# Optimization experiments

Hardware: AMD Instinct MI355X
Metric: run time of the kernel (lower is better)

## Reference

```python
import jax, jax.numpy as jnp
import numpy as np

N = 50000   # nodes
E = 600000  # edges (avg degree 12)
D = 128     # feature dim (input=hidden=output)
L = 3       # GIN layers
BN_EPS = 1e-5


def _bn(x, g, b):
    # BatchNorm1d in training mode: per-feature batch mean / biased variance
    m = jnp.mean(x, axis=0)
    v = jnp.var(x, axis=0)
    return (x - m) * jax.lax.rsqrt(v + BN_EPS) * g + b


def setup_inputs() -> dict:
    key = jax.random.key(0)
    ks = jax.random.split(key, 5)
    h = jax.random.normal(ks[0], (N, D), jnp.float32)
    edges = jax.random.randint(ks[1], (2, E), 0, N, dtype=jnp.int32)
    w = jax.random.uniform(ks[2], (E,), jnp.float32)
    scale = 1.0 / np.sqrt(D)
    W0s = jax.random.normal(ks[3], (L, D, D), jnp.float32) * scale
    W1s = jax.random.normal(ks[4], (L, D, D), jnp.float32) * scale
    ones = jnp.ones((L, D), jnp.float32)
    zeros = jnp.zeros((L, D), jnp.float32)
    return dict(h=h, edges=edges, w=w, W0s=W0s, W1s=W1s,
                bn1_g=ones, bn1_b=zeros,   # MLP internal BN
                bn2_g=ones, bn2_b=zeros,   # ApplyNodeFunc BN
                bn3_g=ones, bn3_b=zeros)   # outer GIN BN


def reference(h, edges, w, W0s, W1s, bn1_g, bn1_b, bn2_g, bn2_b, bn3_g, bn3_b):
    src, dst = edges[0], edges[1]
    for i in range(L):
        # GINConv, sum pooling, eps = 0: (1+eps)*h + sum_{j in N(v)} w_ij * h_j
        agg = jax.ops.segment_sum(h[src] * w[:, None], dst, num_segments=N)
        x = h + agg
        # ApplyNodeFunc: MLP (lin -> BN -> relu -> lin), then BN, relu
        x = jax.nn.relu(_bn(x @ W0s[i], bn1_g[i], bn1_b[i]))
        x = x @ W1s[i]
        x = jax.nn.relu(_bn(x, bn2_g[i], bn2_b[i]))
        # outer per-layer BatchNorm; relu except on the last layer
        h = _bn(x, bn3_g[i], bn3_b[i])
        if i != L - 1:
            h = jax.nn.relu(h)
    return h
```

## Files before the change

kernel.cpp:

```cpp
#include <hip/hip_runtime.h>
#include <stdint.h>

#define NN 50000
#define EE 600000
#define DD 128
#define LL 3
#define NB 196
#define NBANK 16
#define SB (NBANK * 256)
#define GA 3125

typedef __attribute__((ext_vector_type(8))) short short8;
typedef __attribute__((ext_vector_type(4))) float f32x4;
typedef __attribute__((ext_vector_type(4))) unsigned int u32x4;

static __device__ __forceinline__ ushort f2bf(float f) {
    uint32_t u = __builtin_bit_cast(uint32_t, f);
    u += 0x7FFFu + ((u >> 16) & 1u);
    return (ushort)(u >> 16);
}
static __device__ __forceinline__ float bf2f(ushort u) {
    uint32_t x = ((uint32_t)u) << 16;
    return __builtin_bit_cast(float, x);
}
static __device__ __forceinline__ float bflo(uint32_t p) { return bf2f((ushort)(p & 0xffffu)); }
static __device__ __forceinline__ float bfhi(uint32_t p) { return bf2f((ushort)(p >> 16)); }

static __device__ __forceinline__ void gload_lds16(const void* g, void* l) {
    __builtin_amdgcn_global_load_lds(
        (const __attribute__((address_space(1))) uint32_t*)g,
        (__attribute__((address_space(3))) uint32_t*)l, 16, 0, 0);
}

static __device__ __forceinline__ float2 bank_sum(const float* st, int t) {
    float s1 = 0.f, s2 = 0.f;
    #pragma unroll
    for (int bb = 0; bb < NBANK; ++bb) {
        s1 += st[bb * 256 + t];
        s2 += st[bb * 256 + DD + t];
    }
    return make_float2(s1, s2);
}

__global__ __launch_bounds__(256) void prep_w(
    const float* __restrict__ W0s, const float* __restrict__ W1s,
    ushort* __restrict__ wt, int* __restrict__ deg, float* __restrict__ stats)
{
    __shared__ float ws[8192];
    const int b = blockIdx.x;
    const int t = threadIdx.x;

    {
        int i = b * 256 + t;
        if (i < NN) deg[i] = 0;
        if (b >= 12 && b < 12 + 9 * NBANK) stats[(b - 12) * 256 + t] = 0.f;
    }

    if (b < 12) {
        const int m = b >> 1, kh = b & 1;
        const float* W = (m < 3 ? W0s + (size_t)m * 16384
                                : W1s + (size_t)(m - 3) * 16384) + (size_t)kh * 64 * 128;
        #pragma unroll
        for (int i = 0; i < 8; ++i) {
            int i4 = t + i * 256;
            reinterpret_cast<float4*>(ws)[i4] = reinterpret_cast<const float4*>(W)[i4];
        }
        __syncthreads();
        ushort* out = wt + (size_t)m * 16384;
        const int j = t & 127;
        const int rep = t >> 7;
        #pragma unroll
        for (int si = 0; si < 4; ++si) {
            int s = kh * 8 + rep * 4 + si;
            int kloc = (rep * 4 + si) * 8;
            short8 pk;
            #pragma unroll
            for (int q = 0; q < 8; ++q) pk[q] = (short)f2bf(ws[(kloc + q) * 128 + j]);
            int slot = s ^ (j & 7);
            *reinterpret_cast<short8*>(out + j * 128 + slot * 8) = pk;
        }
    }
}

__global__ __launch_bounds__(256) void hist_kernel(
    const int* __restrict__ dst, int* __restrict__ deg)
{
    int e = blockIdx.x * 256 + threadIdx.x;
    if (e < EE) atomicAdd(&deg[dst[e]], 1);
}

__global__ __launch_bounds__(256) void scan_a(
    const int* __restrict__ deg, int* __restrict__ partials)
{
    int i = blockIdx.x * 256 + threadIdx.x;
    int v = (i < NN) ? deg[i] : 0;
    #pragma unroll
    for (int d = 1; d < 64; d <<= 1) v += __shfl_xor(v, d);
    __shared__ int wsum[4];
    if ((threadIdx.x & 63) == 0) wsum[threadIdx.x >> 6] = v;
    __syncthreads();
    if (threadIdx.x == 0)
        partials[blockIdx.x] = wsum[0] + wsum[1] + wsum[2] + wsum[3];
}

__global__ __launch_bounds__(256) void scan_c(
    const int* __restrict__ deg, const int* __restrict__ partials,
    int* __restrict__ off, int* __restrict__ cursor)
{
    __shared__ int ps[256], s[256];
    const int t = threadIdx.x;
    int pv = (t < NB) ? partials[t] : 0;
    ps[t] = pv;
    __syncthreads();
    for (int d = 1; d < 256; d <<= 1) {
        int u = (t >= d) ? ps[t - d] : 0;
        __syncthreads();
        ps[t] += u;
        __syncthreads();
    }
    int base = (blockIdx.x > 0) ? ps[blockIdx.x - 1] : 0;

    int i = blockIdx.x * 256 + t;
    int v = (i < NN) ? deg[i] : 0;
    s[t] = v;
    __syncthreads();
    for (int d = 1; d < 256; d <<= 1) {
        int u = (t >= d) ? s[t - d] : 0;
        __syncthreads();
        s[t] += u;
        __syncthreads();
    }
    int excl = base + s[t] - v;
    if (i < NN) { off[i] = excl; cursor[i] = excl; }
    if (i == 0) off[NN] = EE;
}

__global__ __launch_bounds__(256) void binsort_kernel(
    const int* __restrict__ src, const int* __restrict__ dst,
    const float* __restrict__ w, int* __restrict__ cursor,
    int2* __restrict__ em)
{
    int e = blockIdx.x * 256 + threadIdx.x;
    if (e >= EE) return;
    int d = dst[e];
    int p = atomicAdd(&cursor[d], 1);
    em[p] = make_int2(src[e], __float_as_int(w[e]));
}

__global__ __launch_bounds__(256) void gather_kernel(
    const ushort* __restrict__ y0, const int* __restrict__ off,
    const long long* __restrict__ em, ushort* __restrict__ y,
    float* __restrict__ st0)
{
    __shared__ float red[4][256];
    const int t = threadIdx.x;
    const int wave = t >> 6, lane = t & 63;
    const int qw = lane >> 4, ql = lane & 15;
    const int v = blockIdx.x * 16 + wave * 4 + qw;

    const int beg = off[v], end = off[v + 1];
    const ushort* rowbase = y0 + ql * 8;

    uint4 sw = *reinterpret_cast<const uint4*>(y0 + (size_t)v * DD + ql * 8);
    float a0 = bflo(sw.x), a1 = bfhi(sw.x), a2 = bflo(sw.y), a3 = bfhi(sw.y);
    float a4 = bflo(sw.z), a5 = bfhi(sw.z), a6 = bflo(sw.w), a7 = bfhi(sw.w);

    int j = beg;
    for (; j + 3 < end; j += 4) {
        long long q0 = __builtin_nontemporal_load(&em[j]);
        long long q1 = __builtin_nontemporal_load(&em[j + 1]);
        long long q2 = __builtin_nontemporal_load(&em[j + 2]);
        long long q3 = __builtin_nontemporal_load(&em[j + 3]);
        int s0 = (int)(q0 & 0xffffffffLL), s1 = (int)(q1 & 0xffffffffLL);
        int s2 = (int)(q2 & 0xffffffffLL), s3 = (int)(q3 & 0xffffffffLL);
        float w0 = __int_as_float((int)(q0 >> 32)), w1 = __int_as_float((int)(q1 >> 32));
        float w2 = __int_as_float((int)(q2 >> 32)), w3 = __int_as_float((int)(q3 >> 32));
        uint4 p0 = *reinterpret_cast<const uint4*>(rowbase + (size_t)s0 * DD);
        uint4 p1 = *reinterpret_cast<const uint4*>(rowbase + (size_t)s1 * DD);
        uint4 p2 = *reinterpret_cast<const uint4*>(rowbase + (size_t)s2 * DD);
        uint4 p3 = *reinterpret_cast<const uint4*>(rowbase + (size_t)s3 * DD);
        a0 = fmaf(w0, bflo(p0.x), a0); a1 = fmaf(w0, bfhi(p0.x), a1);
        a2 = fmaf(w0, bflo(p0.y), a2); a3 = fmaf(w0, bfhi(p0.y), a3);
        a4 = fmaf(w0, bflo(p0.z), a4); a5 = fmaf(w0, bfhi(p0.z), a5);
        a6 = fmaf(w0, bflo(p0.w), a6); a7 = fmaf(w0, bfhi(p0.w), a7);
        a0 = fmaf(w1, bflo(p1.x), a0); a1 = fmaf(w1, bfhi(p1.x), a1);
        a2 = fmaf(w1, bflo(p1.y), a2); a3 = fmaf(w1, bfhi(p1.y), a3);
        a4 = fmaf(w1, bflo(p1.z), a4); a5 = fmaf(w1, bfhi(p1.z), a5);
        a6 = fmaf(w1, bflo(p1.w), a6); a7 = fmaf(w1, bfhi(p1.w), a7);
        a0 = fmaf(w2, bflo(p2.x), a0); a1 = fmaf(w2, bfhi(p2.x), a1);
        a2 = fmaf(w2, bflo(p2.y), a2); a3 = fmaf(w2, bfhi(p2.y), a3);
        a4 = fmaf(w2, bflo(p2.z), a4); a5 = fmaf(w2, bfhi(p2.z), a5);
        a6 = fmaf(w2, bflo(p2.w), a6); a7 = fmaf(w2, bfhi(p2.w), a7);
        a0 = fmaf(w3, bflo(p3.x), a0); a1 = fmaf(w3, bfhi(p3.x), a1);
        a2 = fmaf(w3, bflo(p3.y), a2); a3 = fmaf(w3, bfhi(p3.y), a3);
        a4 = fmaf(w3, bflo(p3.z), a4); a5 = fmaf(w3, bfhi(p3.z), a5);
        a6 = fmaf(w3, bflo(p3.w), a6); a7 = fmaf(w3, bfhi(p3.w), a7);
    }
    for (; j < end; ++j) {
        long long q0 = __builtin_nontemporal_load(&em[j]);
        int s0 = (int)(q0 & 0xffffffffLL);
        float w0 = __int_as_float((int)(q0 >> 32));
        uint4 p0 = *reinterpret_cast<const uint4*>(rowbase + (size_t)s0 * DD);
        a0 = fmaf(w0, bflo(p0.x), a0); a1 = fmaf(w0, bfhi(p0.x), a1);
        a2 = fmaf(w0, bflo(p0.y), a2); a3 = fmaf(w0, bfhi(p0.y), a3);
        a4 = fmaf(w0, bflo(p0.z), a4); a5 = fmaf(w0, bfhi(p0.z), a5);
        a6 = fmaf(w0, bflo(p0.w), a6); a7 = fmaf(w0, bfhi(p0.w), a7);
    }
    ushort r0 = f2bf(a0), r1 = f2bf(a1), r2 = f2bf(a2), r3 = f2bf(a3);
    ushort r4 = f2bf(a4), r5 = f2bf(a5), r6 = f2bf(a6), r7 = f2bf(a7);
    u32x4 ow;
    ow.x = (uint32_t)r0 | ((uint32_t)r1 << 16);
    ow.y = (uint32_t)r2 | ((uint32_t)r3 << 16);
    ow.z = (uint32_t)r4 | ((uint32_t)r5 << 16);
    ow.w = (uint32_t)r6 | ((uint32_t)r7 << 16);
    __builtin_nontemporal_store(ow, reinterpret_cast<u32x4*>(y + (size_t)v * DD + ql * 8));

    float b[8], q[8];
    b[0] = bf2f(r0); b[1] = bf2f(r1); b[2] = bf2f(r2); b[3] = bf2f(r3);
    b[4] = bf2f(r4); b[5] = bf2f(r5); b[6] = bf2f(r6); b[7] = bf2f(r7);
    #pragma unroll
    for (int k = 0; k < 8; ++k) {
        q[k] = b[k] * b[k];
        b[k] += __shfl_xor(b[k], 16); q[k] += __shfl_xor(q[k], 16);
        b[k] += __shfl_xor(b[k], 32); q[k] += __shfl_xor(q[k], 32);
    }
    if (qw == 0) {
        #pragma unroll
        for (int k = 0; k < 8; ++k) {
            red[wave][ql * 8 + k] = b[k];
            red[wave][128 + ql * 8 + k] = q[k];
        }
    }
    __syncthreads();
    if (t < 128) {
        float s1 = red[0][t] + red[1][t] + red[2][t] + red[3][t];
        float s2 = red[0][128 + t] + red[1][128 + t] + red[2][128 + t] + red[3][128 + t];
        float* stb = st0 + (blockIdx.x & (NBANK - 1)) * 256;
        atomicAdd(&stb[t], s1);
        atomicAdd(&stb[DD + t], s2);
    }
}

template <int MODE>
__global__ __launch_bounds__(256) void gemm_mfma(
    const float* __restrict__ in_f,
    const ushort* __restrict__ in_h,
    const ushort* __restrict__ wt,
    const float* __restrict__ stP, const float* __restrict__ gP, const float* __restrict__ bP,
    const float* __restrict__ stQ, const float* __restrict__ gQ, const float* __restrict__ bQ,
    ushort* __restrict__ out,
    float* __restrict__ stats)
{
    __shared__ ushort WT[16384];
    __shared__ float scP[DD], shP[DD], scQ[DD], shQ[DD];

    const int t = threadIdx.x;
    const int lane = t & 63;
    const int wave = t >> 6;

    if (MODE >= 1 && t < DD) {
        float2 s12 = bank_sum(stP, t);
        float m = s12.x * (1.0f / NN);
        float var = s12.y * (1.0f / NN) - m * m;
        float s = gP[t] * rsqrtf(var + 1e-5f);
        scP[t] = s;
        shP[t] = fmaf(-m, s, bP[t]);
    }
    if (MODE == 1 && t < DD) {
        float2 s12 = bank_sum(stQ, t);
        float m = s12.x * (1.0f / NN);
        float var = s12.y * (1.0f / NN) - m * m;
        float s = gQ[t] * rsqrtf(var + 1e-5f);
        scQ[t] = s;
        shQ[t] = fmaf(-m, s, bQ[t]);
    }

    #pragma unroll
    for (int i = 0; i < 8; ++i) {
        int chunk = i * 4 + wave;
        gload_lds16(wt + (size_t)chunk * 512 + lane * 8, WT + chunk * 512);
    }
    __syncthreads();

    const int rgrp = wave >> 1;
    const int chalf = wave & 1;
    const int l15 = lane & 15, lg = lane >> 4;

    short8 Bf[4][4];
    #pragma unroll
    for (int jt = 0; jt < 4; ++jt) {
        int j = chalf * 64 + jt * 16 + l15;
        #pragma unroll
        for (int kk = 0; kk < 4; ++kk) {
            int slot = (kk * 4 + lg) ^ (j & 7);
            Bf[jt][kk] = *reinterpret_cast<const short8*>(WT + j * 128 + slot * 8);
        }
    }

    ushort (*Cst)[136] = reinterpret_cast<ushort(*)[136]>(WT);

    float psum[4] = {0.f, 0.f, 0.f, 0.f};
    float psq[4]  = {0.f, 0.f, 0.f, 0.f};

    #pragma unroll 1
    for (int s = 0; s < 4; ++s) {
        const int row0 = blockIdx.x * 128 + rgrp * 64 + s * 16;
        const bool active = row0 < NN;
        f32x4 acc[4] = {};

        if (active) {
            int row = row0 + l15;
            short8 Af[4];
            #pragma unroll
            for (int kk = 0; kk < 4; ++kk) {
                int kb = kk * 32 + lg * 8;
                float v[8];
                if (MODE == 0) {
                    const float* xr = in_f + (size_t)row * DD + kb;
                    float4 a0 = reinterpret_cast<const float4*>(xr)[0];
                    float4 a1 = reinterpret_cast<const float4*>(xr)[1];
                    v[0]=a0.x; v[1]=a0.y; v[2]=a0.z; v[3]=a0.w;
                    v[4]=a1.x; v[5]=a1.y; v[6]=a1.z; v[7]=a1.w;
                } else {
                    short8 raw = *reinterpret_cast<const short8*>(in_h + (size_t)row * DD + kb);
                    #pragma unroll
                    for (int q = 0; q < 8; ++q) v[q] = bf2f((ushort)raw[q]);
                    float4 p0 = *reinterpret_cast<const float4*>(&scP[kb]);
                    float4 p1 = *reinterpret_cast<const float4*>(&scP[kb + 4]);
                    float4 h0 = *reinterpret_cast<const float4*>(&shP[kb]);
                    float4 h1 = *reinterpret_cast<const float4*>(&shP[kb + 4]);
                    v[0]=fmaxf(fmaf(v[0],p0.x,h0.x),0.f);
                    v[1]=fmaxf(fmaf(v[1],p0.y,h0.y),0.f);
                    v[2]=fmaxf(fmaf(v[2],p0.z,h0.z),0.f);
                    v[3]=fmaxf(fmaf(v[3],p0.w,h0.w),0.f);
                    v[4]=fmaxf(fmaf(v[4],p1.x,h1.x),0.f);
                    v[5]=fmaxf(fmaf(v[5],p1.y,h1.y),0.f);
                    v[6]=fmaxf(fmaf(v[6],p1.z,h1.z),0.f);
                    v[7]=fmaxf(fmaf(v[7],p1.w,h1.w),0.f);
                    if (MODE == 1) {
                        float4 q0v = *reinterpret_cast<const float4*>(&scQ[kb]);
                        float4 q1v = *reinterpret_cast<const float4*>(&scQ[kb + 4]);
                        float4 r0v = *reinterpret_cast<const float4*>(&shQ[kb]);
                        float4 r1v = *reinterpret_cast<const float4*>(&shQ[kb + 4]);
                        v[0]=fmaxf(fmaf(v[0],q0v.x,r0v.x),0.f);
                        v[1]=fmaxf(fmaf(v[1],q0v.y,r0v.y),0.f);
                        v[2]=fmaxf(fmaf(v[2],q0v.z,r0v.z),0.f);
                        v[3]=fmaxf(fmaf(v[3],q0v.w,r0v.w),0.f);
                        v[4]=fmaxf(fmaf(v[4],q1v.x,r1v.x),0.f);
                        v[5]=fmaxf(fmaf(v[5],q1v.y,r1v.y),0.f);
                        v[6]=fmaxf(fmaf(v[6],q1v.z,r1v.z),0.f);
                        v[7]=fmaxf(fmaf(v[7],q1v.w,r1v.w),0.f);
                    }
                }
                short8 af;
                #pragma unroll
                for (int q = 0; q < 8; ++q) af[q] = (short)f2bf(v[q]);
                Af[kk] = af;
            }

            #pragma unroll
            for (int jt = 0; jt < 4; ++jt)
                #pragma unroll
                for (int kk = 0; kk < 4; ++kk)
                    acc[jt] = __builtin_amdgcn_mfma_f32_16x16x32_bf16(
                        Af[kk], Bf[jt][kk], acc[jt], 0, 0, 0);

            if (MODE == 2) {
                #pragma unroll
                for (int jt = 0; jt < 4; ++jt)
                    #pragma unroll
                    for (int i = 0; i < 4; ++i) {
                        float val = acc[jt][i];
                        psum[jt] += val;
                        psq[jt] += val * val;
                    }
            }
        }

        __syncthreads();
        if (active) {
            #pragma unroll
            for (int jt = 0; jt < 4; ++jt) {
                int col = chalf * 64 + jt * 16 + l15;
                #pragma unroll
                for (int i = 0; i < 4; ++i)
                    Cst[rgrp * 16 + lg * 4 + i][col] = f2bf(acc[jt][i]);
            }
        }
        __syncthreads();
        {
            int r = t >> 3, cg2 = t & 7;
            int lrow = (r < 16) ? (s * 16 + r) : (64 + s * 16 + (r - 16));
            int grow = blockIdx.x * 128 + lrow;
            if (grow < NN) {
                short8 v0 = *reinterpret_cast<const short8*>(&Cst[r][cg2 * 16]);
                short8 v1 = *reinterpret_cast<const short8*>(&Cst[r][cg2 * 16 + 8]);
                *reinterpret_cast<short8*>(out + (size_t)grow * DD + cg2 * 16) = v0;
                *reinterpret_cast<short8*>(out + (size_t)grow * DD + cg2 * 16 + 8) = v1;
            }
        }
    }

    if (MODE == 2) {
        float* stb = stats + (blockIdx.x & (NBANK - 1)) * 256;
        #pragma unroll
        for (int jt = 0; jt < 4; ++jt) {
            float s1 = psum[jt], s2 = psq[jt];
            s1 += __shfl_xor(s1, 16); s2 += __shfl_xor(s2, 16);
            s1 += __shfl_xor(s1, 32); s2 += __shfl_xor(s2, 32);
            if (lg == 0) {
                int f = chalf * 64 + jt * 16 + l15;
                atomicAdd(&stb[f], s1);
                atomicAdd(&stb[DD + f], s2);
            }
        }
    }
}

__global__ __launch_bounds__(256) void stats_relu(
    const ushort* __restrict__ z, const float* __restrict__ stin,
    const float* __restrict__ g, const float* __restrict__ b,
    float* __restrict__ stats)
{
    __shared__ float ssum[DD], ssq[DD], sc[DD], sh[DD];
    int t = threadIdx.x;
    if (t < DD) {
        ssum[t] = 0.f; ssq[t] = 0.f;
        float2 s12 = bank_sum(stin, t);
        float m = s12.x * (1.0f / NN);
        float var = s12.y * (1.0f / NN) - m * m;
        float s = g[t] * rsqrtf(var + 1e-5f);
        sc[t] = s;
        sh[t] = fmaf(-m, s, b[t]);
    }
    __syncthreads();

    int f = (t * 4) & 127;
    float4 scv = *reinterpret_cast<const float4*>(&sc[f]);
    float4 shv = *reinterpret_cast<const float4*>(&sh[f]);
    float p0=0,p1=0,p2=0,p3=0,q0=0,q1=0,q2=0,q3=0;
    size_t stride = (size_t)gridDim.x * 1024;
    for (size_t idx = (size_t)blockIdx.x * 1024 + t * 4; idx < (size_t)NN * DD; idx += stride) {
        uint2 zz = *reinterpret_cast<const uint2*>(z + idx);
        float u0 = fmaxf(fmaf(bflo(zz.x), scv.x, shv.x), 0.f);
        float u1 = fmaxf(fmaf(bfhi(zz.x), scv.y, shv.y), 0.f);
        float u2 = fmaxf(fmaf(bflo(zz.y), scv.z, shv.z), 0.f);
        float u3 = fmaxf(fmaf(bfhi(zz.y), scv.w, shv.w), 0.f);
        p0 += u0; q0 += u0 * u0;
        p1 += u1; q1 += u1 * u1;
        p2 += u2; q2 += u2 * u2;
        p3 += u3; q3 += u3 * u3;
    }
    atomicAdd(&ssum[f + 0], p0); atomicAdd(&ssq[f + 0], q0);
    atomicAdd(&ssum[f + 1], p1); atomicAdd(&ssq[f + 1], q1);
    atomicAdd(&ssum[f + 2], p2); atomicAdd(&ssq[f + 2], q2);
    atomicAdd(&ssum[f + 3], p3); atomicAdd(&ssq[f + 3], q3);
    __syncthreads();
    float* stb = stats + (blockIdx.x & (NBANK - 1)) * 256;
    if (t < DD) {
        atomicAdd(&stb[t], ssum[t]);
        atomicAdd(&stb[DD + t], ssq[t]);
    }
}

__global__ __launch_bounds__(256) void final_apply(
    const ushort* __restrict__ z,
    const float* __restrict__ st2in, const float* __restrict__ g2,
    const float* __restrict__ b2,
    const float* __restrict__ st3in, const float* __restrict__ g3,
    const float* __restrict__ b3,
    float* __restrict__ out)
{
    __shared__ float sc2[DD], sh2[DD], sc3[DD], sh3[DD];
    int t = threadIdx.x;
    if (t < DD) {
        float2 s12 = bank_sum(st2in, t);
        float m = s12.x * (1.0f / NN);
        float var = s12.y * (1.0f / NN) - m * m;
        float s = g2[t] * rsqrtf(var + 1e-5f);
        sc2[t] = s;
        sh2[t] = fmaf(-m, s, b2[t]);
        s12 = bank_sum(st3in, t);
        m = s12.x * (1.0f / NN);
        var = s12.y * (1.0f / NN) - m * m;
        s = g3[t] * rsqrtf(var + 1e-5f);
        sc3[t] = s;
        sh3[t] = fmaf(-m, s, b3[t]);
    }
    __syncthreads();

    int f = (t * 4) & 127;
    float4 s2 = *reinterpret_cast<const float4*>(&sc2[f]);
    float4 h2 = *reinterpret_cast<const float4*>(&sh2[f]);
    float4 s3 = *reinterpret_cast<const float4*>(&sc3[f]);
    float4 h3 = *reinterpret_cast<const float4*>(&sh3[f]);
    size_t stride = (size_t)gridDim.x * 1024;
    for (size_t idx = (size_t)blockIdx.x * 1024 + t * 4; idx < (size_t)NN * DD; idx += stride) {
        uint2 zz = *reinterpret_cast<const uint2*>(z + idx);
        float4 o;
        float u;
        u = fmaxf(fmaf(bflo(zz.x), s2.x, h2.x), 0.f); o.x = fmaf(u, s3.x, h3.x);
        u = fmaxf(fmaf(bfhi(zz.x), s2.y, h2.y), 0.f); o.y = fmaf(u, s3.y, h3.y);
        u = fmaxf(fmaf(bflo(zz.y), s2.z, h2.z), 0.f); o.z = fmaf(u, s3.z, h3.z);
        u = fmaxf(fmaf(bfhi(zz.y), s2.w, h2.w), 0.f); o.w = fmaf(u, s3.w, h3.w);
        *reinterpret_cast<float4*>(out + idx) = o;
    }
}

extern "C" void kernel_launch(void* const* d_in, const int* in_sizes, int n_in,
                              void* d_out, int out_size, void* d_ws, size_t ws_size,
                              hipStream_t stream)
{
    const float* h0   = (const float*)d_in[0];
    const int*  edges = (const int*)d_in[1];
    const float* w    = (const float*)d_in[2];
    const float* W0s  = (const float*)d_in[3];
    const float* W1s  = (const float*)d_in[4];
    const float* bn1g = (const float*)d_in[5];
    const float* bn1b = (const float*)d_in[6];
    const float* bn2g = (const float*)d_in[7];
    const float* bn2b = (const float*)d_in[8];
    const float* bn3g = (const float*)d_in[9];
    const float* bn3b = (const float*)d_in[10];
    float* out = (float*)d_out;

    const size_t ND = (size_t)NN * DD;
    ushort* y0buf = (ushort*)d_ws;
    ushort* ybuf  = y0buf + ND;
    ushort* zbuf  = ybuf + ND;
    ushort* wtbuf = zbuf + ND;
    float*  stats = (float*)(wtbuf + 6 * 16384);
    int*    deg      = (int*)(stats + 9 * SB);
    int*    off      = deg + NN;
    int*    cursor   = off + NN + 1;
    int*    partials = cursor + NN + 1;
    int2*   em       = (int2*)(partials + NB + 2);

    const int* src = edges;
    const int* dst = edges + EE;

    prep_w<<<NB, 256, 0, stream>>>(W0s, W1s, wtbuf, deg, stats);
    hist_kernel<<<(EE + 255) / 256, 256, 0, stream>>>(dst, deg);
    scan_a<<<NB, 256, 0, stream>>>(deg, partials);
    scan_c<<<NB, 256, 0, stream>>>(deg, partials, off, cursor);
    binsort_kernel<<<(EE + 255) / 256, 256, 0, stream>>>(src, dst, w, cursor, em);

    const int GG = (NN + 127) / 128;

    for (int i = 0; i < LL; ++i) {
        float* st0 = stats + (i * 3 + 0) * SB;
        float* st1 = stats + (i * 3 + 1) * SB;
        float* st2 = stats + (i * 3 + 2) * SB;
        const ushort* wt0 = wtbuf + (size_t)i * 16384;
        const ushort* wt1 = wtbuf + (size_t)(i + 3) * 16384;

        if (i == 0) {
            gemm_mfma<0><<<GG, 256, 0, stream>>>(
                h0, nullptr, wt0,
                nullptr, nullptr, nullptr, nullptr, nullptr, nullptr,
                y0buf, nullptr);
        } else {
            float* st1p = stats + ((i - 1) * 3 + 1) * SB;
            float* st2p = stats + ((i - 1) * 3 + 2) * SB;
            gemm_mfma<1><<<GG, 256, 0, stream>>>(
                nullptr, zbuf, wt0,
                st1p, bn2g + (i - 1) * DD, bn2b + (i - 1) * DD,
                st2p, bn3g + (i - 1) * DD, bn3b + (i - 1) * DD,
                y0buf, nullptr);
        }

        gather_kernel<<<GA, 256, 0, stream>>>(y0buf, off, (const long long*)em, ybuf, st0);

        gemm_mfma<2><<<GG, 256, 0, stream>>>(
            nullptr, ybuf, wt1,
            st0, bn1g + i * DD, bn1b + i * DD,
            nullptr, nullptr, nullptr,
            zbuf, st1);

        stats_relu<<<1024, 256, 0, stream>>>(zbuf, st1, bn2g + i * DD, bn2b + i * DD, st2);
    }

    final_apply<<<2048, 256, 0, stream>>>(
        zbuf,
        stats + (2 * 3 + 1) * SB, bn2g + 2 * DD, bn2b + 2 * DD,
        stats + (2 * 3 + 2) * SB, bn3g + 2 * DD, bn3b + 2 * DD,
        out);
}
```

Baseline: 290.8 us.

## Replace per-node atomic binsort with two-stage bucketed counting sort

Edges are sorted by destination in two passes instead of one. The first pass buckets them into 256-node buckets using shared-memory counts and one global atomic per bucket per block, writing to a staging buffer with dst and src packed into 32 bits. The second pass scatters each bucket into final CSR order using shared-memory cursors. This removes about 600k contended global atomics and random scatter writes, at the cost of one extra kernel launch and an extra pass over a staging buffer.

```diff
diff --git a/kernel.cpp b/kernel.cpp
--- a/kernel.cpp
+++ b/kernel.cpp
@@ -6,9 +6,12 @@
 #define DD 128
 #define LL 3
 #define NB 196
+#define NBKT 196
 #define NBANK 16
 #define SB (NBANK * 256)
 #define GA 3125
+#define B1CH 2048
+#define B1G ((EE + B1CH - 1) / B1CH)
 
 typedef __attribute__((ext_vector_type(8))) short short8;
 typedef __attribute__((ext_vector_type(4))) float f32x4;
@@ -105,7 +108,7 @@
 
 __global__ __launch_bounds__(256) void scan_c(
     const int* __restrict__ deg, const int* __restrict__ partials,
-    int* __restrict__ off, int* __restrict__ cursor)
+    int* __restrict__ off, int* __restrict__ bcur)
 {
     __shared__ int ps[256], s[256];
     const int t = threadIdx.x;
@@ -131,20 +134,69 @@
         __syncthreads();
     }
     int excl = base + s[t] - v;
-    if (i < NN) { off[i] = excl; cursor[i] = excl; }
+    if (i < NN) {
+        off[i] = excl;
+        if ((i & 255) == 0) bcur[i >> 8] = excl;
+    }
     if (i == 0) off[NN] = EE;
 }
 
-__global__ __launch_bounds__(256) void binsort_kernel(
+__global__ __launch_bounds__(256) void bin_stage1(
     const int* __restrict__ src, const int* __restrict__ dst,
-    const float* __restrict__ w, int* __restrict__ cursor,
+    const float* __restrict__ w, int* __restrict__ bcur,
+    int2* __restrict__ stg)
+{
+    __shared__ int cnt[NBKT], gb[NBKT];
+    const int t = threadIdx.x;
+    const int e0 = blockIdx.x * B1CH;
+    for (int b = t; b < NBKT; b += 256) cnt[b] = 0;
+    __syncthreads();
+    #pragma unroll
+    for (int k = 0; k < B1CH / 256; ++k) {
+        int e = e0 + k * 256 + t;
+        if (e < EE) atomicAdd(&cnt[dst[e] >> 8], 1);
+    }
+    __syncthreads();
+    for (int b = t; b < NBKT; b += 256) {
+        int c = cnt[b];
+        if (c > 0) gb[b] = atomicAdd(&bcur[b], c);
+        cnt[b] = 0;
+    }
+    __syncthreads();
+    #pragma unroll
+    for (int k = 0; k < B1CH / 256; ++k) {
+        int e = e0 + k * 256 + t;
+        if (e < EE) {
+            int d = dst[e];
+            int b = d >> 8;
+            int p = gb[b] + atomicAdd(&cnt[b], 1);
+            stg[p] = make_int2((d << 16) | src[e], __float_as_int(w[e]));
+        }
+    }
+}
+
+__global__ __launch_bounds__(256) void bin_stage2(
+    const int* __restrict__ off, const int2* __restrict__ stg,
     int2* __restrict__ em)
 {
-    int e = blockIdx.x * 256 + threadIdx.x;
-    if (e >= EE) return;
-    int d = dst[e];
-    int p = atomicAdd(&cursor[d], 1);
-    em[p] = make_int2(src[e], __float_as_int(w[e]));
+    __shared__ int lcur[256];
+    const int t = threadIdx.x;
+    const int b = blockIdx.x;
+    const int n0 = b * 256;
+    int nidx = n0 + t;
+    lcur[t] = (nidx < NN) ? off[nidx] : EE;
+    int hi = n0 + 256; if (hi > NN) hi = NN;
+    const int rbeg = off[n0];
+    const int rend = off[hi];
+    __syncthreads();
+    for (int p = rbeg + t; p < rend; p += 256) {
+        int2 en = stg[p];
+        uint32_t key = (uint32_t)en.x;
+        int d_local = (int)(key >> 16) & 255;
+        int srcv = (int)(key & 0xffffu);
+        int pos = atomicAdd(&lcur[d_local], 1);
+        em[pos] = make_int2(srcv, en.y);
+    }
 }
 
 __global__ __launch_bounds__(256) void gather_kernel(
@@ -532,9 +584,10 @@
     float*  stats = (float*)(wtbuf + 6 * 16384);
     int*    deg      = (int*)(stats + 9 * SB);
     int*    off      = deg + NN;
-    int*    cursor   = off + NN + 1;
-    int*    partials = cursor + NN + 1;
+    int*    bcur     = off + NN + 1;
+    int*    partials = bcur + NBKT;
     int2*   em       = (int2*)(partials + NB + 2);
+    int2*   stg      = em + EE;
 
     const int* src = edges;
     const int* dst = edges + EE;
@@ -542,8 +595,9 @@
     prep_w<<<NB, 256, 0, stream>>>(W0s, W1s, wtbuf, deg, stats);
     hist_kernel<<<(EE + 255) / 256, 256, 0, stream>>>(dst, deg);
     scan_a<<<NB, 256, 0, stream>>>(deg, partials);
-    scan_c<<<NB, 256, 0, stream>>>(deg, partials, off, cursor);
-    binsort_kernel<<<(EE + 255) / 256, 256, 0, stream>>>(src, dst, w, cursor, em);
+    scan_c<<<NB, 256, 0, stream>>>(deg, partials, off, bcur);
+    bin_stage1<<<B1G, 256, 0, stream>>>(src, dst, w, bcur, stg);
+    bin_stage2<<<NBKT, 256, 0, stream>>>(off, stg, em);
 
     const int GG = (NN + 127) / 128;
 
```

Result: faster. 284.4 us (median of 2 runs) (-2.2%).
